# Optimization experiments

Hardware: AMD Instinct MI355X
Metric: run time of the kernel (lower is better)

Reference implementation:

```python
import jax, jax.numpy as jnp
import numpy as np

SWITCH_W = 30.0
TOL = 5
DECAY = 0.7
FP_PEN = 10.0
INV_PEN = 100.0
CLASS_W = jnp.array([1.0, 1.0, SWITCH_W, SWITCH_W], dtype=jnp.float32)


def setup_inputs() -> dict:
    key = jax.random.key(0)
    k1, k2, k3 = jax.random.split(key, 3)
    B, S, C = 512, 8192, 4
    logits = jax.random.normal(k1, (B, S, C), dtype=jnp.float32)
    labels = jax.random.randint(k2, (B, S), 0, 4, dtype=jnp.int32)
    # sprinkle ignore_index (-100) positions like real padded sequences
    drop = jax.random.uniform(k3, (B, S)) < 0.05
    labels = jnp.where(drop, jnp.int32(-100), labels)
    return {"logits": logits, "labels": labels}


def _mode_multiplier(labels, preds):
    """Sequential state machine over time; carry = (pred_mode, true_mode) per batch row."""
    B, S = labels.shape

    def step(carry, xs):
        pm, tm = carry
        lab, pred = xs  # [B] each
        valid = lab != -100
        # invalid transition penalty on predicted switches
        bad = ((pred == 2) & (pm == 0)) | ((pred == 3) & (pm == 1))
        pen = jnp.where(valid & bad, INV_PEN, 1.0)
        new_pm = jnp.where(valid, jnp.where((pred == 0) | (pred == 2), 0, 1), pm)
        # reward correct mode switches (true label agrees with pred switch)
        good = ((lab == 2) & (tm == 1) & (pred == 2)) | ((lab == 3) & (tm == 0) & (pred == 3))
        bonus = jnp.where(valid & good, 0.1, 1.0)
        new_tm = jnp.where(valid & ((lab == 0) | (lab == 2)), 0,
                           jnp.where(valid & ((lab == 1) | (lab == 3)), 1, tm))
        return (new_pm, new_tm), pen * bonus

    init = (jnp.zeros((B,), jnp.int32), jnp.zeros((B,), jnp.int32))
    _, mult = jax.lax.scan(step, init, (labels.T, preds.T))
    return mult.T  # [B, S]


def _nearest_dist(mask):
    """For each position, distance to nearest True in the same row; BIG if none."""
    B, S = mask.shape
    BIG = jnp.int32(S + TOL + 2)

    def f(c, m):
        c = jnp.where(m, jnp.int32(0), jnp.minimum(c + 1, BIG))
        return c, c

    init = jnp.full((B,), BIG, jnp.int32)
    _, fwd = jax.lax.scan(f, init, mask.T)
    _, bwd = jax.lax.scan(f, init, mask[:, ::-1].T)
    return jnp.minimum(fwd.T, bwd.T[:, ::-1])


def _loss(logits, labels):
    preds = jnp.argmax(logits, axis=-1).astype(jnp.int32)
    valid = labels != -100
    labs = jnp.where(valid, labels, 0)
    logp = jax.nn.log_softmax(logits, axis=-1)
    ce = -jnp.take_along_axis(logp, labs[..., None], axis=-1)[..., 0] * CLASS_W[labs]

    mult = _mode_multiplier(labels, preds)
    for c in (2, 3):
        true_m = labels == c
        pred_m = preds == c
        d_true = _nearest_dist(true_m)
        d_pred = _nearest_dist(pred_m)
        has_true = true_m.any(axis=1, keepdims=True)
        has_pred = pred_m.any(axis=1, keepdims=True)
        # multipliers at predicted-switch positions
        mp = jnp.where(
            pred_m,
            jnp.where(
                has_true,
                jnp.where(d_true == 0, 0.1,
                          jnp.where(d_true <= TOL, DECAY ** d_true.astype(jnp.float32), FP_PEN)),
                FP_PEN * 2.0),
            1.0)
        # multipliers at true-switch positions
        mt = jnp.where(
            true_m,
            jnp.where(has_pred, jnp.where(d_pred > TOL, 2.0, 1.0), 3.0),
            1.0)
        mult = mult * mp * mt

    vf = valid.astype(ce.dtype)
    total = (ce * mult * vf).sum()
    return total / jnp.maximum(vf.sum(), 1.0)


def reference(logits, labels):
    return _loss(logits, labels)
```

## Files before the change

kernel.cpp:

```cpp
#include <hip/hip_runtime.h>
#include <math.h>

#define BROWS 512
#define SLEN  8192
#define NT    1024
#define CHUNK (SLEN / NT)
#define NWRD  (SLEN / 32)
#define MWRD  (NWRD + 2)

__device__ __forceinline__ int win_dist(const unsigned int* __restrict__ M, int t) {
    int sI = t + 27;
    int w  = sI >> 5;
    int off = sI & 31;
    unsigned long long val =
        ((unsigned long long)M[w] | ((unsigned long long)M[w + 1] << 32)) >> off;
    unsigned int win = (unsigned int)val & 0x7FFu;
    if (win & 32u) return 0;
    unsigned int dn = win & 31u;
    unsigned int up = (win >> 6) & 31u;
    int d = 99;
    if (dn) d = 5 - (31 - __clz((int)dn));
    if (up) { int du = __ffs((int)up); if (du < d) d = du; }
    return d;
}

__device__ __forceinline__ float decay_pow(int d) {
    return (d == 1) ? 0.7f : (d == 2) ? 0.49f : (d == 3) ? 0.343f
         : (d == 4) ? 0.2401f : 0.16807f;
}

__global__ __launch_bounds__(NT, 8) void row_loss_kernel(
    const float* __restrict__ logits, const int* __restrict__ labels,
    double* __restrict__ psum, unsigned int* __restrict__ pcnt)
{
    __shared__ float         s_ce[SLEN];
    __shared__ unsigned char s_pk[SLEN];
    __shared__ unsigned int  s_m[4][MWRD];
    __shared__ unsigned int  s_wave[16];
    __shared__ unsigned int  s_wavex[16];
    __shared__ unsigned int  s_flags;
    __shared__ double        s_red[16];
    __shared__ int           s_redc[16];

    const int row  = blockIdx.x;
    const int tid  = threadIdx.x;
    const int lane = tid & 63;
    const int wid  = tid >> 6;

    if (tid < 8) s_m[tid >> 1][(tid & 1) ? (MWRD - 1) : 0] = 0u;
    if (tid == 0) s_flags = 0u;

    const float4* lg4 = (const float4*)(logits + (size_t)row * SLEN * 4);
    const int*    lb  = labels + (size_t)row * SLEN;

    int cnt = 0;
    #pragma unroll
    for (int kk = 0; kk < CHUNK; kk += 4) {
        float4 v[4]; int la[4];
        #pragma unroll
        for (int j = 0; j < 4; ++j) {
            int t = (kk + j) * NT + tid;
            v[j]  = lg4[t];
            la[j] = lb[t];
        }
        #pragma unroll
        for (int j = 0; j < 4; ++j) {
            int t = (kk + j) * NT + tid;
            float4 q = v[j];
            int lab  = la[j];
            float m01 = fmaxf(q.x, q.y), m23 = fmaxf(q.z, q.w);
            float best = fmaxf(m01, m23);
            int pred = (best == q.x) ? 0 : (best == q.y) ? 1 : (best == q.z) ? 2 : 3;
            bool valid = (lab != -100);
            cnt += valid ? 1 : 0;
            int l = valid ? (lab & 3) : 0;
            float se = __expf(q.x - best) + __expf(q.y - best) +
                       __expf(q.z - best) + __expf(q.w - best);
            float lse = best + __logf(se);
            float xl = (l == 0) ? q.x : (l == 1) ? q.y : (l == 2) ? q.z : q.w;
            float wc = (l >= 2) ? 30.0f : 1.0f;
            s_ce[t] = valid ? (lse - xl) * wc : 0.0f;
            s_pk[t] = (unsigned char)(pred | (l << 2) | (valid ? 16 : 0));
        }
    }
    __syncthreads();

    const int base = tid * CHUNK;
    const unsigned long long pkw = *(const unsigned long long*)(s_pk + base);
    unsigned int mt2 = 0, mp2 = 0, mt3 = 0, mp3 = 0;
    unsigned int summary = 0;
    #pragma unroll
    for (int i = 0; i < CHUNK; ++i) {
        unsigned int pk = (unsigned int)(pkw >> (8 * i)) & 31u;
        int pred = pk & 3, l = (pk >> 2) & 3;
        bool valid = (pk & 16) != 0;
        if (pred == 2) mp2 |= 1u << i;
        if (pred == 3) mp3 |= 1u << i;
        if (valid && l == 2) mt2 |= 1u << i;
        if (valid && l == 3) mt3 |= 1u << i;
        if (valid) summary = 4u | (unsigned)(pred & 1) | ((unsigned)(l & 1) << 1);
    }
    {
        int sh = (tid & 3) * 8;
        unsigned int w0 = mt2 << sh, w1 = mp2 << sh, w2 = mt3 << sh, w3 = mp3 << sh;
        w0 |= __shfl_xor(w0, 1); w0 |= __shfl_xor(w0, 2);
        w1 |= __shfl_xor(w1, 1); w1 |= __shfl_xor(w1, 2);
        w2 |= __shfl_xor(w2, 1); w2 |= __shfl_xor(w2, 2);
        w3 |= __shfl_xor(w3, 1); w3 |= __shfl_xor(w3, 2);
        if ((tid & 3) == 0) {
            int wi = 1 + (tid >> 2);
            s_m[0][wi] = w0; s_m[1][wi] = w1; s_m[2][wi] = w2; s_m[3][wi] = w3;
        }
    }
    {
        unsigned int fl = (mt2 ? 1u : 0u) | (mp2 ? 2u : 0u) |
                          (mt3 ? 4u : 0u) | (mp3 ? 8u : 0u);
        #pragma unroll
        for (int s = 32; s > 0; s >>= 1) fl |= __shfl_xor(fl, s);
        if (lane == 0 && fl) atomicOr(&s_flags, fl);
    }

    unsigned int inc = summary;
    #pragma unroll
    for (int st = 1; st < 64; st <<= 1) {
        unsigned int o = __shfl_up(inc, st);
        if (lane >= st && !(inc & 4u)) inc = o;
    }
    unsigned int exc = __shfl_up(inc, 1);
    if (lane == 0) exc = 0u;
    if (lane == 63) s_wave[wid] = inc;
    __syncthreads();
    if (wid == 0) {
        unsigned int wv = (lane < 16) ? s_wave[lane] : 0u;
        #pragma unroll
        for (int st = 1; st < 16; st <<= 1) {
            unsigned int o = __shfl_up(wv, st);
            if (lane >= st && !(wv & 4u)) wv = o;
        }
        unsigned int wex = __shfl_up(wv, 1);
        if (lane == 0) wex = 0u;
        if (lane < 16) s_wavex[lane] = wex;
    }
    __syncthreads();

    unsigned int pre = (exc & 4u) ? exc : s_wavex[wid];
    int pm = (int)(pre & 1u), tm = (int)((pre >> 1) & 1u);
    const unsigned int flags = s_flags;
    const bool hasT2 = flags & 1u, hasP2 = flags & 2u;
    const bool hasT3 = flags & 4u, hasP3 = flags & 8u;

    float4 c0 = *(const float4*)(s_ce + base);
    float4 c1 = *(const float4*)(s_ce + base + 4);
    float cearr[8] = {c0.x, c0.y, c0.z, c0.w, c1.x, c1.y, c1.z, c1.w};

    float acc = 0.0f;
    #pragma unroll
    for (int i = 0; i < CHUNK; ++i) {
        int t = base + i;
        unsigned int pk = (unsigned int)(pkw >> (8 * i)) & 31u;
        int pred = pk & 3, l = (pk >> 2) & 3;
        bool valid = (pk & 16) != 0;
        float m = 1.0f;
        if (valid) {
            bool bad = (pred == 2 && pm == 0) || (pred == 3 && pm == 1);
            if (bad) m *= 100.0f;
            bool good = (l == 2 && tm == 1 && pred == 2) ||
                        (l == 3 && tm == 0 && pred == 3);
            if (good) m *= 0.1f;
            pm = pred & 1;
            tm = l & 1;
        }
        if (pred >= 2) {
            bool has = (pred == 2) ? hasT2 : hasT3;
            if (!has) m *= 20.0f;
            else {
                int d = win_dist(s_m[(pred - 2) << 1], t);
                m *= (d == 0) ? 0.1f : (d <= 5) ? decay_pow(d) : 10.0f;
            }
        }
        if (valid && l >= 2) {
            bool has = (l == 2) ? hasP2 : hasP3;
            if (!has) m *= 3.0f;
            else if (win_dist(s_m[1 + ((l - 2) << 1)], t) > 5) m *= 2.0f;
        }
        acc += cearr[i] * m;
    }

    double dacc = (double)acc;
    #pragma unroll
    for (int o = 32; o > 0; o >>= 1) {
        dacc += __shfl_down(dacc, o);
        cnt  += __shfl_down(cnt, o);
    }
    if (lane == 0) { s_red[wid] = dacc; s_redc[wid] = cnt; }
    __syncthreads();
    if (tid == 0) {
        double tot = 0.0; unsigned int c = 0;
        #pragma unroll
        for (int i = 0; i < 16; ++i) { tot += s_red[i]; c += (unsigned int)s_redc[i]; }
        psum[row] = tot;
        pcnt[row] = c;
    }
}

__global__ __launch_bounds__(512) void finalize_kernel(
    const double* __restrict__ psum, const unsigned int* __restrict__ pcnt,
    float* __restrict__ out)
{
    __shared__ double       sd[8];
    __shared__ unsigned int sc[8];
    int tid = threadIdx.x, lane = tid & 63, wid = tid >> 6;
    double v = psum[tid];
    unsigned int c = pcnt[tid];
    #pragma unroll
    for (int o = 32; o > 0; o >>= 1) {
        v += __shfl_down(v, o);
        c += __shfl_down(c, o);
    }
    if (lane == 0) { sd[wid] = v; sc[wid] = c; }
    __syncthreads();
    if (tid == 0) {
        double t = 0.0; unsigned int cc = 0;
        #pragma unroll
        for (int i = 0; i < 8; ++i) { t += sd[i]; cc += sc[i]; }
        double d = (cc > 0u) ? (double)cc : 1.0;
        out[0] = (float)(t / d);
    }
}

extern "C" void kernel_launch(void* const* d_in, const int* in_sizes, int n_in,
                              void* d_out, int out_size, void* d_ws, size_t ws_size,
                              hipStream_t stream) {
    const float* logits = (const float*)d_in[0];
    const int*   labels = (const int*)d_in[1];
    float* out = (float*)d_out;
    double* psum = (double*)d_ws;
    unsigned int* pcnt = (unsigned int*)(psum + BROWS);

    row_loss_kernel<<<BROWS, NT, 0, stream>>>(logits, labels, psum, pcnt);
    finalize_kernel<<<1, 512, 0, stream>>>(psum, pcnt, out);
}
```

Before: 112.8 us.

## Build switch bitmasks via ballots during load and drop a block barrier

Builds the per-class switch bitmasks with wave ballots inside the load loop, in place of a second pass over packed bytes followed by shuffles. Per-wave flag words replace the shared atomicOr. The cross-wave prefix scan done by wave 0 is replaced by each wave serially reading earlier wave summaries, which removes one __syncthreads. Logits and labels are read with nontemporal loads. The trade-off is extra ballot instructions and shared stores in the memory-bound load phase, plus a small serial loop per wave.

Result: slower. 118.8 us (+5.3%).

```diff
diff --git a/kernel.cpp b/kernel.cpp
--- a/kernel.cpp
+++ b/kernel.cpp
@@ -7,6 +7,8 @@
 #define CHUNK (SLEN / NT)
 #define NWRD  (SLEN / 32)
 #define MWRD  (NWRD + 2)
+
+typedef float f32x4v __attribute__((ext_vector_type(4)));
 
 __device__ __forceinline__ int win_dist(const unsigned int* __restrict__ M, int t) {
     int sI = t + 27;
@@ -37,8 +39,7 @@
     __shared__ unsigned char s_pk[SLEN];
     __shared__ unsigned int  s_m[4][MWRD];
     __shared__ unsigned int  s_wave[16];
-    __shared__ unsigned int  s_wavex[16];
-    __shared__ unsigned int  s_flags;
+    __shared__ unsigned int  s_wfl[16];
     __shared__ double        s_red[16];
     __shared__ int           s_redc[16];
 
@@ -46,80 +47,70 @@
     const int tid  = threadIdx.x;
     const int lane = tid & 63;
     const int wid  = tid >> 6;
+    const int half = lane >> 5;
 
     if (tid < 8) s_m[tid >> 1][(tid & 1) ? (MWRD - 1) : 0] = 0u;
-    if (tid == 0) s_flags = 0u;
-
-    const float4* lg4 = (const float4*)(logits + (size_t)row * SLEN * 4);
+
+    const f32x4v* lgv = (const f32x4v*)(logits + (size_t)row * SLEN * 4);
     const int*    lb  = labels + (size_t)row * SLEN;
 
     int cnt = 0;
+    unsigned int wfl = 0u;
     #pragma unroll
     for (int kk = 0; kk < CHUNK; kk += 4) {
-        float4 v[4]; int la[4];
+        f32x4v v[4]; int la[4];
         #pragma unroll
         for (int j = 0; j < 4; ++j) {
             int t = (kk + j) * NT + tid;
-            v[j]  = lg4[t];
-            la[j] = lb[t];
+            v[j]  = __builtin_nontemporal_load(lgv + t);
+            la[j] = __builtin_nontemporal_load(lb + t);
         }
         #pragma unroll
         for (int j = 0; j < 4; ++j) {
             int t = (kk + j) * NT + tid;
-            float4 q = v[j];
+            f32x4v q = v[j];
             int lab  = la[j];
-            float m01 = fmaxf(q.x, q.y), m23 = fmaxf(q.z, q.w);
+            float m01 = fmaxf(q[0], q[1]), m23 = fmaxf(q[2], q[3]);
             float best = fmaxf(m01, m23);
-            int pred = (best == q.x) ? 0 : (best == q.y) ? 1 : (best == q.z) ? 2 : 3;
+            int pred = (best == q[0]) ? 0 : (best == q[1]) ? 1 : (best == q[2]) ? 2 : 3;
             bool valid = (lab != -100);
             cnt += valid ? 1 : 0;
             int l = valid ? (lab & 3) : 0;
-            float se = __expf(q.x - best) + __expf(q.y - best) +
-                       __expf(q.z - best) + __expf(q.w - best);
+            float se = __expf(q[0] - best) + __expf(q[1] - best) +
+                       __expf(q[2] - best) + __expf(q[3] - best);
             float lse = best + __logf(se);
-            float xl = (l == 0) ? q.x : (l == 1) ? q.y : (l == 2) ? q.z : q.w;
+            float xl = (l == 0) ? q[0] : (l == 1) ? q[1] : (l == 2) ? q[2] : q[3];
             float wc = (l >= 2) ? 30.0f : 1.0f;
             s_ce[t] = valid ? (lse - xl) * wc : 0.0f;
             s_pk[t] = (unsigned char)(pred | (l << 2) | (valid ? 16 : 0));
-        }
-    }
+
+            unsigned long long bt2 = __ballot(valid && l == 2);
+            unsigned long long bp2 = __ballot(pred == 2);
+            unsigned long long bt3 = __ballot(valid && l == 3);
+            unsigned long long bp3 = __ballot(pred == 3);
+            wfl |= (bt2 ? 1u : 0u) | (bp2 ? 2u : 0u) |
+                   (bt3 ? 4u : 0u) | (bp3 ? 8u : 0u);
+            if ((lane & 31) == 0) {
+                int wi = 1 + (kk + j) * 32 + (wid << 1) + half;
+                unsigned int sh = (unsigned int)(half << 5);
+                s_m[0][wi] = (unsigned int)(bt2 >> sh);
+                s_m[1][wi] = (unsigned int)(bp2 >> sh);
+                s_m[2][wi] = (unsigned int)(bt3 >> sh);
+                s_m[3][wi] = (unsigned int)(bp3 >> sh);
+            }
+        }
+    }
+    if (lane == 0) s_wfl[wid] = wfl;
     __syncthreads();
 
     const int base = tid * CHUNK;
     const unsigned long long pkw = *(const unsigned long long*)(s_pk + base);
-    unsigned int mt2 = 0, mp2 = 0, mt3 = 0, mp3 = 0;
     unsigned int summary = 0;
     #pragma unroll
     for (int i = 0; i < CHUNK; ++i) {
         unsigned int pk = (unsigned int)(pkw >> (8 * i)) & 31u;
-        int pred = pk & 3, l = (pk >> 2) & 3;
-        bool valid = (pk & 16) != 0;
-        if (pred == 2) mp2 |= 1u << i;
-        if (pred == 3) mp3 |= 1u << i;
-        if (valid && l == 2) mt2 |= 1u << i;
-        if (valid && l == 3) mt3 |= 1u << i;
-        if (valid) summary = 4u | (unsigned)(pred & 1) | ((unsigned)(l & 1) << 1);
-    }
-    {
-        int sh = (tid & 3) * 8;
-        unsigned int w0 = mt2 << sh, w1 = mp2 << sh, w2 = mt3 << sh, w3 = mp3 << sh;
-        w0 |= __shfl_xor(w0, 1); w0 |= __shfl_xor(w0, 2);
-        w1 |= __shfl_xor(w1, 1); w1 |= __shfl_xor(w1, 2);
-        w2 |= __shfl_xor(w2, 1); w2 |= __shfl_xor(w2, 2);
-        w3 |= __shfl_xor(w3, 1); w3 |= __shfl_xor(w3, 2);
-        if ((tid & 3) == 0) {
-            int wi = 1 + (tid >> 2);
-            s_m[0][wi] = w0; s_m[1][wi] = w1; s_m[2][wi] = w2; s_m[3][wi] = w3;
-        }
-    }
-    {
-        unsigned int fl = (mt2 ? 1u : 0u) | (mp2 ? 2u : 0u) |
-                          (mt3 ? 4u : 0u) | (mp3 ? 8u : 0u);
-        #pragma unroll
-        for (int s = 32; s > 0; s >>= 1) fl |= __shfl_xor(fl, s);
-        if (lane == 0 && fl) atomicOr(&s_flags, fl);
-    }
-
+        if (pk & 16u) summary = 4u | (pk & 1u) | ((pk >> 1) & 2u);
+    }
     unsigned int inc = summary;
     #pragma unroll
     for (int st = 1; st < 64; st <<= 1) {
@@ -130,28 +121,24 @@
     if (lane == 0) exc = 0u;
     if (lane == 63) s_wave[wid] = inc;
     __syncthreads();
-    if (wid == 0) {
-        unsigned int wv = (lane < 16) ? s_wave[lane] : 0u;
-        #pragma unroll
-        for (int st = 1; st < 16; st <<= 1) {
-            unsigned int o = __shfl_up(wv, st);
-            if (lane >= st && !(wv & 4u)) wv = o;
-        }
-        unsigned int wex = __shfl_up(wv, 1);
-        if (lane == 0) wex = 0u;
-        if (lane < 16) s_wavex[lane] = wex;
-    }
-    __syncthreads();
-
-    unsigned int pre = (exc & 4u) ? exc : s_wavex[wid];
+
+    unsigned int wpre = 0u;
+    for (int k = 0; k < wid; ++k) {
+        unsigned int w = s_wave[k];
+        if (w & 4u) wpre = w;
+    }
+    unsigned int flags = 0u;
+    #pragma unroll
+    for (int k = 0; k < 16; ++k) flags |= s_wfl[k];
+
+    unsigned int pre = (exc & 4u) ? exc : wpre;
     int pm = (int)(pre & 1u), tm = (int)((pre >> 1) & 1u);
-    const unsigned int flags = s_flags;
     const bool hasT2 = flags & 1u, hasP2 = flags & 2u;
     const bool hasT3 = flags & 4u, hasP3 = flags & 8u;
 
-    float4 c0 = *(const float4*)(s_ce + base);
-    float4 c1 = *(const float4*)(s_ce + base + 4);
-    float cearr[8] = {c0.x, c0.y, c0.z, c0.w, c1.x, c1.y, c1.z, c1.w};
+    f32x4v c0 = *(const f32x4v*)(s_ce + base);
+    f32x4v c1 = *(const f32x4v*)(s_ce + base + 4);
+    float cearr[8] = {c0[0], c0[1], c0[2], c0[3], c1[0], c1[1], c1[2], c1[3]};
 
     float acc = 0.0f;
     #pragma unroll
```
